# Performance work log

Measured on AMD Instinct MI355X. Metric: run time of the kernel, lower is better.

## Reference

```python
import jax, jax.numpy as jnp
import numpy as np
from jax import lax

H = 32  # hidden_dim

def _lstm_layer(x_tbd, W_ih, W_hh, b_ih, b_hh):
    """x_tbd: [T, B, D]. Returns all hidden states [T, B, H]. PyTorch gate order i,f,g,o."""
    T, B, _ = x_tbd.shape
    # Precompute input contribution for all timesteps (one big GEMM)
    xW = jnp.einsum('tbd,gd->tbg', x_tbd, W_ih) + (b_ih + b_hh)  # [T, B, 4H]
    W_hh_T = W_hh.T  # [H, 4H]

    def step(carry, xw):
        h, c = carry
        gates = xw + h @ W_hh_T  # [B, 4H]
        i, f, g, o = jnp.split(gates, 4, axis=-1)
        i = jax.nn.sigmoid(i)
        f = jax.nn.sigmoid(f)
        g = jnp.tanh(g)
        o = jax.nn.sigmoid(o)
        c = f * c + i * g
        h = o * jnp.tanh(c)
        return (h, c), h

    h0 = jnp.zeros((B, H), x_tbd.dtype)
    (_, _), hs = lax.scan(step, (h0, h0), xW)
    return hs  # [T, B, H]


def setup_inputs() -> dict:
    key = jax.random.key(0)
    ks = jax.random.split(key, 12)
    s = 0.1  # keep gates out of saturation
    return {
        'x': jax.random.normal(ks[0], (4096, 512, 4), jnp.float32),
        'W_ih0': jax.random.normal(ks[1], (4 * H, 4), jnp.float32) * s,
        'W_hh0': jax.random.normal(ks[2], (4 * H, H), jnp.float32) * s,
        'b_ih0': jax.random.normal(ks[3], (4 * H,), jnp.float32) * s,
        'b_hh0': jax.random.normal(ks[4], (4 * H,), jnp.float32) * s,
        'W_ih1': jax.random.normal(ks[5], (4 * H, H), jnp.float32) * s,
        'W_hh1': jax.random.normal(ks[6], (4 * H, H), jnp.float32) * s,
        'b_ih1': jax.random.normal(ks[7], (4 * H,), jnp.float32) * s,
        'b_hh1': jax.random.normal(ks[8], (4 * H,), jnp.float32) * s,
        'W_out': jax.random.normal(ks[9], (1, H), jnp.float32) * s,
        'b_out': jax.random.normal(ks[10], (1,), jnp.float32) * s,
    }


def reference(x, W_ih0, W_hh0, b_ih0, b_hh0, W_ih1, W_hh1, b_ih1, b_hh1, W_out, b_out):
    # x: [B, T, D] (batch_first). Eval mode -> inter-layer dropout is identity.
    x_tbd = jnp.transpose(x, (1, 0, 2))  # [T, B, D]
    h1 = _lstm_layer(x_tbd, W_ih0, W_hh0, b_ih0, b_hh0)  # [T, B, H]
    h2 = _lstm_layer(h1, W_ih1, W_hh1, b_ih1, b_hh1)     # [T, B, H]
    last = h2[-1]  # [B, H] == out[:, -1, :]
    return last @ W_out.T + b_out  # [B, 1]
```

## Files before the change

### kernel.cpp

```cpp
#include <hip/hip_runtime.h>
#include <cmath>

constexpr int T   = 512;
constexpr int D   = 4;
constexpr int H   = 32;
constexpr int BT  = 16;
constexpr int BLK = 256;

constexpr float LOG2E     = 1.44269504088896340736f;
constexpr float NEG2LOG2E = -2.88539008177792681472f;

constexpr int XSTRIDE = 4104;
constexpr int HSTR = 40;

typedef short bf8 __attribute__((ext_vector_type(8)));
typedef short s4v __attribute__((ext_vector_type(4)));
typedef float f4  __attribute__((ext_vector_type(4)));
typedef float f2  __attribute__((ext_vector_type(2)));

static __device__ __forceinline__ short bf16_rtn(float v) {
    unsigned u = __float_as_uint(v);
    u += 0x7FFFu + ((u >> 16) & 1u);
    return (short)(u >> 16);
}

__global__ __launch_bounds__(BLK, 1) void lstm_bf16p(
    const float* __restrict__ x,
    const float* __restrict__ W_ih0, const float* __restrict__ W_hh0,
    const float* __restrict__ b_ih0, const float* __restrict__ b_hh0,
    const float* __restrict__ W_ih1, const float* __restrict__ W_hh1,
    const float* __restrict__ b_ih1, const float* __restrict__ b_hh1,
    const float* __restrict__ W_out, const float* __restrict__ b_out,
    float* __restrict__ out)
{
    __shared__ __align__(16) short xbf[16 * XSTRIDE];
    __shared__ __align__(16) short h0b[2][16][HSTR];
    __shared__ __align__(16) short h1b[2][16][HSTR];
    __shared__ __align__(16) float h1f[16][36];

    const int tid   = threadIdx.x;
    const int w     = tid >> 6;
    const int lane  = tid & 63;
    const int q     = lane >> 4;
    const int nl    = lane & 15;
    const int layer = w >> 1;
    const int ug    = (w & 1) << 4;
    const int b0    = blockIdx.x * BT;

    for (int idx = tid; idx < 16 * T; idx += BLK) {
        const int col = idx & 15;
        const int t   = idx >> 4;
        float4 xv = *(const float4*)(x + ((size_t)(b0 + col) * T + t) * D);
        bf8 v = {0, 0, 0, 0, 0, 0, 0, 0};
        v[0] = bf16_rtn(xv.x); v[1] = bf16_rtn(xv.y);
        v[2] = bf16_rtn(xv.z); v[3] = bf16_rtn(xv.w);
        *(bf8*)&xbf[col * XSTRIDE + t * 8] = v;
    }
    for (int idx = tid; idx < 2 * 16 * HSTR; idx += BLK) {
        (&h0b[0][0][0])[idx] = 0;
        (&h1b[0][0][0])[idx] = 0;
    }

    const float* W1 = layer ? W_ih1 : W_hh0;
    bf8 w1[4], w2[4];
    f4  bias[4];
    #pragma unroll
    for (int g = 0; g < 4; ++g) {
        const float sc = (g == 2) ? NEG2LOG2E : -LOG2E;
        const int row = 32 * g + ug + nl;
        #pragma unroll
        for (int j = 0; j < 8; ++j) {
            w1[g][j] = bf16_rtn(W1[row * H + 8 * q + j] * sc);
            float v2 = layer ? W_hh1[row * H + 8 * q + j]
                             : ((q == 0 && j < 4) ? W_ih0[row * D + j] : 0.0f);
            w2[g][j] = bf16_rtn(v2 * sc);
        }
        #pragma unroll
        for (int r = 0; r < 4; ++r) {
            const int gr = 32 * g + ug + 4 * q + r;
            bias[g][r] = sc * (layer ? (b_ih1[gr] + b_hh1[gr])
                                     : (b_ih0[gr] + b_hh0[gr]));
        }
    }

    f2 cA; cA.x = 0.0f; cA.y = 0.0f;
    f2 cB; cB.x = 0.0f; cB.y = 0.0f;

    const short* xcol = &xbf[nl * XSTRIDE];

    __syncthreads();

    auto actpair = [&](f2& c2, float zi0, float zi1, float zf0, float zf1,
                       float zg0, float zg1, float zo0, float zo1,
                       unsigned& pkd, f2& hv) {
        f2 ei, ef, eg, eo, ec;
        ei.x = __builtin_amdgcn_exp2f(zi0); ei.y = __builtin_amdgcn_exp2f(zi1);
        ef.x = __builtin_amdgcn_exp2f(zf0); ef.y = __builtin_amdgcn_exp2f(zf1);
        eg.x = __builtin_amdgcn_exp2f(zg0); eg.y = __builtin_amdgcn_exp2f(zg1);
        eo.x = __builtin_amdgcn_exp2f(zo0); eo.y = __builtin_amdgcn_exp2f(zo1);
        f2 D1 = 1.0f + ef;
        f2 D2 = (1.0f + ei) * (1.0f + eg);
        f2 Dm = D1 * D2;
        float R = __builtin_amdgcn_rcpf(Dm.x * Dm.y);
        f2 rD; rD.x = R * Dm.y; rD.y = R * Dm.x;
        c2 = (c2 * D2 + (1.0f - eg) * D1) * rD;
        ec.x = __builtin_amdgcn_exp2f(c2.x * NEG2LOG2E);
        ec.y = __builtin_amdgcn_exp2f(c2.y * NEG2LOG2E);
        f2 Do = (1.0f + eo) * (1.0f + ec);
        float Ro = __builtin_amdgcn_rcpf(Do.x * Do.y);
        f2 ro; ro.x = Ro * Do.y; ro.y = Ro * Do.x;
        hv = (1.0f - ec) * ro;
        asm("v_cvt_pk_bf16_f32 %0, %1, %2" : "=v"(pkd) : "v"(hv.x), "v"(hv.y));
    };

    auto body = [&](const int i, const int rb, const int wb) {
        bf8 b2;
        if (layer == 0) {
            b2 = *(const bf8*)&xcol[(i & (T - 1)) * 8];
        } else {
            b2 = *(const bf8*)&h1b[rb][nl][8 * q];
        }
        bf8 b1 = *(const bf8*)&h0b[rb][nl][8 * q];

        f4 acc[4];
        #pragma unroll
        for (int g = 0; g < 4; ++g) {
            f4 A = __builtin_amdgcn_mfma_f32_16x16x32_bf16(w2[g], b2, bias[g], 0, 0, 0);
            A    = __builtin_amdgcn_mfma_f32_16x16x32_bf16(w1[g], b1, A,       0, 0, 0);
            acc[g] = A;
        }

        const bool act = layer ? (i >= 1) : (i < T);
        if (act) {
            unsigned pk0, pk1;
            f2 hvA, hvB;
            actpair(cA, acc[0][0], acc[0][1], acc[1][0], acc[1][1],
                        acc[2][0], acc[2][1], acc[3][0], acc[3][1], pk0, hvA);
            actpair(cB, acc[0][2], acc[0][3], acc[1][2], acc[1][3],
                        acc[2][2], acc[2][3], acc[3][2], acc[3][3], pk1, hvB);
            int2 hh; hh.x = (int)pk0; hh.y = (int)pk1;
            if (layer == 0) {
                *(int2*)&h0b[wb][nl][ug + 4 * q] = hh;
            } else {
                *(int2*)&h1b[wb][nl][ug + 4 * q] = hh;
                if (i == T) {
                    float4 hw;
                    hw.x = hvA.x; hw.y = hvA.y; hw.z = hvB.x; hw.w = hvB.y;
                    *(float4*)&h1f[nl][ug + 4 * q] = hw;
                }
            }
        }
        __syncthreads();
    };

    #pragma unroll 1
    for (int i = 0; i < T; i += 2) {
        body(i,     0, 1);
        body(i + 1, 1, 0);
    }
    body(T, 0, 1);

    if (tid < BT) {
        float acc = b_out[0];
        #pragma unroll
        for (int u = 0; u < H; ++u) acc = fmaf(W_out[u], h1f[tid][u], acc);
        out[b0 + tid] = acc;
    }
}

extern "C" void kernel_launch(void* const* d_in, const int* in_sizes, int n_in,
                              void* d_out, int out_size, void* d_ws, size_t ws_size,
                              hipStream_t stream) {
    const float* x     = (const float*)d_in[0];
    const float* W_ih0 = (const float*)d_in[1];
    const float* W_hh0 = (const float*)d_in[2];
    const float* b_ih0 = (const float*)d_in[3];
    const float* b_hh0 = (const float*)d_in[4];
    const float* W_ih1 = (const float*)d_in[5];
    const float* W_hh1 = (const float*)d_in[6];
    const float* b_ih1 = (const float*)d_in[7];
    const float* b_hh1 = (const float*)d_in[8];
    const float* W_out = (const float*)d_in[9];
    const float* b_out = (const float*)d_in[10];
    float* out = (float*)d_out;

    const int B = out_size;
    lstm_bf16p<<<B / BT, BLK, 0, stream>>>(x, W_ih0, W_hh0, b_ih0, b_hh0,
                                           W_ih1, W_hh1, b_ih1, b_hh1,
                                           W_out, b_out, out);
}
```

Baseline: 277.4 us.

## Double the block's wavefronts and split the activation work across wave pairs

The block grows from 4 to 8 wavefronts, so each (layer, unit-group) pair has two waves. Both waves run the same MFMAs, and each one then computes activations for only half of the accumulator rows, writing a packed bf16 pair instead of four values. The aim is to halve the serial transcendental work per wave on the recurrence's critical path and to give more latency hiding. The cost is duplicated MFMA work, twice as many waves in each __syncthreads barrier, and a higher register and occupancy footprint.

```diff
diff --git a/kernel.cpp b/kernel.cpp
--- a/kernel.cpp
+++ b/kernel.cpp
@@ -5,7 +5,7 @@
 constexpr int D   = 4;
 constexpr int H   = 32;
 constexpr int BT  = 16;
-constexpr int BLK = 256;
+constexpr int BLK = 512;
 
 constexpr float LOG2E     = 1.44269504088896340736f;
 constexpr float NEG2LOG2E = -2.88539008177792681472f;
@@ -14,7 +14,6 @@
 constexpr int HSTR = 40;
 
 typedef short bf8 __attribute__((ext_vector_type(8)));
-typedef short s4v __attribute__((ext_vector_type(4)));
 typedef float f4  __attribute__((ext_vector_type(4)));
 typedef float f2  __attribute__((ext_vector_type(2)));
 
@@ -43,8 +42,10 @@
     const int lane  = tid & 63;
     const int q     = lane >> 4;
     const int nl    = lane & 15;
-    const int layer = w >> 1;
-    const int ug    = (w & 1) << 4;
+    const int rsel  = w >> 2;
+    const int wl    = w & 3;
+    const int layer = wl >> 1;
+    const int ug    = (wl & 1) << 4;
     const int b0    = blockIdx.x * BT;
 
     for (int idx = tid; idx < 16 * T; idx += BLK) {
@@ -83,14 +84,13 @@
         }
     }
 
-    f2 cA; cA.x = 0.0f; cA.y = 0.0f;
-    f2 cB; cB.x = 0.0f; cB.y = 0.0f;
+    f2 c2; c2.x = 0.0f; c2.y = 0.0f;
 
     const short* xcol = &xbf[nl * XSTRIDE];
 
     __syncthreads();
 
-    auto actpair = [&](f2& c2, float zi0, float zi1, float zf0, float zf1,
+    auto actpair = [&](float zi0, float zi1, float zf0, float zf1,
                        float zg0, float zg1, float zo0, float zo1,
                        unsigned& pkd, f2& hv) {
         f2 ei, ef, eg, eo, ec;
@@ -132,22 +132,19 @@
 
         const bool act = layer ? (i >= 1) : (i < T);
         if (act) {
-            unsigned pk0, pk1;
-            f2 hvA, hvB;
-            actpair(cA, acc[0][0], acc[0][1], acc[1][0], acc[1][1],
-                        acc[2][0], acc[2][1], acc[3][0], acc[3][1], pk0, hvA);
-            actpair(cB, acc[0][2], acc[0][3], acc[1][2], acc[1][3],
-                        acc[2][2], acc[2][3], acc[3][2], acc[3][3], pk1, hvB);
-            int2 hh; hh.x = (int)pk0; hh.y = (int)pk1;
-            if (layer == 0) {
-                *(int2*)&h0b[wb][nl][ug + 4 * q] = hh;
+            unsigned pk; f2 hv;
+            if (rsel == 0) {
+                actpair(acc[0][0], acc[0][1], acc[1][0], acc[1][1],
+                        acc[2][0], acc[2][1], acc[3][0], acc[3][1], pk, hv);
             } else {
-                *(int2*)&h1b[wb][nl][ug + 4 * q] = hh;
-                if (i == T) {
-                    float4 hw;
-                    hw.x = hvA.x; hw.y = hvA.y; hw.z = hvB.x; hw.w = hvB.y;
-                    *(float4*)&h1f[nl][ug + 4 * q] = hw;
-                }
+                actpair(acc[0][2], acc[0][3], acc[1][2], acc[1][3],
+                        acc[2][2], acc[2][3], acc[3][2], acc[3][3], pk, hv);
+            }
+            short* hb = layer ? &h1b[wb][nl][0] : &h0b[wb][nl][0];
+            *(unsigned*)&hb[ug + 4 * q + 2 * rsel] = pk;
+            if (layer && i == T) {
+                float2 hw; hw.x = hv.x; hw.y = hv.y;
+                *(float2*)&h1f[nl][ug + 4 * q + 2 * rsel] = hw;
             }
         }
         __syncthreads();
```

Measured after the change: 282.5 us. No clear change (+1.9%).
